# Performance work log

Measured on AMD Instinct MI355X. Metric: run time of the kernel, lower is better.

The kernel has to match this reference:

```python
import jax, jax.numpy as jnp
import numpy as np
import math

B, S, HID, H = 8, 512, 1024, 16
D = HID // H
ATT_SPAN = 512  # max_position_embeddings


def setup_inputs() -> dict:
    key = jax.random.key(0)
    ks = jax.random.split(key, 12)
    sd = 0.02
    hidden_states = jax.random.normal(ks[0], (B, S, HID), jnp.float32)
    attention_mask = jnp.zeros((B, 1, 1, S), jnp.float32)
    # DeBERTa build_relative_position: rel[i, j] = i - j, shape [1, 1, S, S]
    rel = (jnp.arange(S)[:, None] - jnp.arange(S)[None, :]).astype(jnp.int32)
    relative_pos = rel[None, None]
    Wq = jax.random.normal(ks[1], (HID, HID), jnp.float32) * sd
    bq = jnp.zeros((HID,), jnp.float32)
    Wk = jax.random.normal(ks[2], (HID, HID), jnp.float32) * sd
    bk = jnp.zeros((HID,), jnp.float32)
    Wv = jax.random.normal(ks[3], (HID, HID), jnp.float32) * sd
    bv = jnp.zeros((HID,), jnp.float32)
    Wpk = jax.random.normal(ks[4], (HID, HID), jnp.float32) * sd
    bpk = jnp.zeros((HID,), jnp.float32)
    rel_emb = jax.random.normal(ks[5], (2 * ATT_SPAN, HID), jnp.float32) * sd
    return dict(hidden_states=hidden_states, attention_mask=attention_mask,
                relative_pos=relative_pos, Wq=Wq, bq=bq, Wk=Wk, bk=bk,
                Wv=Wv, bv=bv, Wpk=Wpk, bpk=bpk, rel_emb=rel_emb)


def _fwd(hidden_states, attention_mask, relative_pos, Wq, bq, Wk, bk, Wv, bv, Wpk, bpk, rel_emb):
    b, s, _ = hidden_states.shape

    def proj(x, W, bias):  # [b,s,hid] -> [b,h,s,d]
        return (x @ W.T + bias).reshape(b, s, H, D).transpose(0, 2, 1, 3)

    q = proj(hidden_states, Wq, bq)
    k = proj(hidden_states, Wk, bk)
    v = proj(hidden_states, Wv, bv)

    # content-to-content scores, scaled by sqrt(3*num_heads) as in source
    s_content = jnp.einsum('bhid,bhjd->bhij', q, k) / math.sqrt(3.0 * H)

    # positional projections (source uses pos_key layer for BOTH key and query)
    # rel_emb: [2*ATT_SPAN, HID] -> [H, 2*ATT_SPAN, D]
    pos = (rel_emb @ Wpk.T + bpk).reshape(2 * ATT_SPAN, H, D).transpose(1, 0, 2)

    # c2p: q @ pos^T / sqrt(all_head_size * 3), then gather along last axis
    c2p_full = jnp.einsum('bhid,hpd->bhip', q, pos) / math.sqrt(HID * 3.0)  # [b,h,s,2P]
    c2p_pos = jnp.clip(relative_pos + ATT_SPAN, 0, 2 * ATT_SPAN - 1)
    c2p_pos = jnp.broadcast_to(c2p_pos, (b, H, s, s)).astype(jnp.int32)
    c2p = jnp.take_along_axis(c2p_full, c2p_pos, axis=-1)  # [b,h,s,s]

    # p2c: pos / sqrt(3*H) @ k^T, gather along dim -2 with same index
    p2c_full = jnp.einsum('hpd,bhjd->bhpj', pos / math.sqrt(3.0 * H), k)  # [b,h,2P,s]
    p2c = jnp.take_along_axis(p2c_full, c2p_pos, axis=-2)  # [b,h,s,s]

    score = s_content + c2p + p2c + attention_mask
    probs = jax.nn.softmax(score, axis=-1)  # dropout is identity in eval
    out = jnp.einsum('bhij,bhjd->bhid', probs, v)
    return out.transpose(0, 2, 1, 3).reshape(b, s, HID)


def reference(hidden_states, attention_mask, relative_pos, Wq, bq, Wk, bk, Wv, bv, Wpk, bpk, rel_emb):
    return _fwd(hidden_states, attention_mask, relative_pos, Wq, bq, Wk, bk, Wv, bv, Wpk, bpk, rel_emb)
```

## Files before the change

kernel.cpp:

```cpp
#include <hip/hip_runtime.h>
#include <cstdint>
#include <cstddef>

static constexpr int NB  = 8;
static constexpr int S   = 512;
static constexpr int HID = 1024;
static constexpr int NH  = 16;
static constexpr int DH  = 64;
static constexpr int P2  = 1024;

static constexpr float INV_S1 = 0.14433756729740643f;

typedef __bf16 v8bf  __attribute__((ext_vector_type(8)));
typedef __bf16 v4bf  __attribute__((ext_vector_type(4)));
typedef float  f32x4 __attribute__((ext_vector_type(4)));

#define MFMA16(acc, a, b) acc = __builtin_amdgcn_mfma_f32_16x16x32_bf16(a, b, acc, 0, 0, 0)

#define GLOAD_LDS16(gp, lp) __builtin_amdgcn_global_load_lds( \
    (const __attribute__((address_space(1))) void*)(gp), \
    (__attribute__((address_space(3))) void*)(lp), 16, 0, 0)

__global__ void castall(const float* __restrict__ x,  const float* __restrict__ wq,
                        const float* __restrict__ wk, const float* __restrict__ wv,
                        const float* __restrict__ wpk, const float* __restrict__ rel,
                        __bf16* __restrict__ ob) {
  size_t e = ((size_t)blockIdx.x * 256 + threadIdx.x) * 4;
  if (e >= 9437184) return;
  const float* src; size_t off;
  if (e < 4194304) { src = x; off = e; }
  else {
    int r = (int)((e - 4194304) >> 20);
    off = (e - 4194304) & 1048575;
    src = (r == 0) ? wq : (r == 1) ? wk : (r == 2) ? wv : (r == 3) ? wpk : rel;
  }
  float4 v = *(const float4*)(src + off);
  v4bf o;
  o[0] = (__bf16)v.x; o[1] = (__bf16)v.y; o[2] = (__bf16)v.z; o[3] = (__bf16)v.w;
  *(v4bf*)(ob + e) = o;
}

__launch_bounds__(256, 4)
__global__ void proj_gemm(const __bf16* __restrict__ Xb, const __bf16* __restrict__ Rb,
                          const __bf16* __restrict__ Wqb, const __bf16* __restrict__ Wkb,
                          const __bf16* __restrict__ Wvb, const __bf16* __restrict__ Wpkb,
                          const float* __restrict__ bq, const float* __restrict__ bk_,
                          const float* __restrict__ bv_, const float* __restrict__ bpk,
                          __bf16* __restrict__ qo, __bf16* __restrict__ ko,
                          __bf16* __restrict__ vto, __bf16* __restrict__ po) {
  const int z = blockIdx.z;
  const __bf16* A; const __bf16* W; const float* bias; __bf16* out; int M; float osc;
  if      (z == 0) { A = Xb; W = Wqb;  bias = bq;  out = qo;  M = 4096; osc = INV_S1; }
  else if (z == 1) { A = Xb; W = Wkb;  bias = bk_; out = ko;  M = 4096; osc = 1.0f; }
  else if (z == 2) { A = Xb; W = Wvb;  bias = bv_; out = vto; M = 4096; osc = 1.0f; }
  else             { A = Rb; W = Wpkb; bias = bpk; out = po;  M = 1024; osc = INV_S1; }
  const int m0 = blockIdx.x * 128;
  if (m0 >= M) return;
  const int n0 = blockIdx.y * 128;
  const int K = 1024;

  __shared__ __bf16 Al[128 * 64];
  __shared__ __bf16 Bl[128 * 64];

  const int t = threadIdx.x;
  const int w = t >> 6, lane = t & 63, q4 = lane >> 4, cc = lane & 15;
  const int wm = w >> 1, wn = w & 1;
  const int srow_in = lane >> 3;
  const int sseg    = ((lane & 7) ^ srow_in) * 8;

  f32x4 acc[4][4] = {};

  for (int k0 = 0; k0 < K; k0 += 64) {
    __syncthreads();
    #pragma unroll
    for (int i = 0; i < 4; i++) {
      int rr = w * 32 + i * 8;
      int gr = rr + srow_in;
      GLOAD_LDS16(&A[(size_t)(m0 + gr) * K + k0 + sseg], &Al[rr * 64]);
      GLOAD_LDS16(&W[(size_t)(n0 + gr) * K + k0 + sseg], &Bl[rr * 64]);
    }
    __syncthreads();
    #pragma unroll
    for (int kk = 0; kk < 2; kk++) {
      v8bf af[4], bfg[4];
      const int phys = ((4 * kk + q4) ^ (cc & 7)) * 8;
      #pragma unroll
      for (int mt = 0; mt < 4; mt++)
        af[mt] = *(const v8bf*)(&Al[(wm * 64 + mt * 16 + cc) * 64 + phys]);
      #pragma unroll
      for (int nt = 0; nt < 4; nt++)
        bfg[nt] = *(const v8bf*)(&Bl[(wn * 64 + nt * 16 + cc) * 64 + phys]);
      #pragma unroll
      for (int mt = 0; mt < 4; mt++)
        #pragma unroll
        for (int nt = 0; nt < 4; nt++)
          MFMA16(acc[mt][nt], af[mt], bfg[nt]);
    }
  }

  #pragma unroll
  for (int mt = 0; mt < 4; mt++) {
    #pragma unroll
    for (int nt = 0; nt < 4; nt++) {
      int n = n0 + wn * 64 + nt * 16 + cc;
      float bsv = bias[n];
      if (z == 2) {
        int m_base = m0 + wm * 64 + mt * 16 + q4 * 4;
        int bb = m_base >> 9, ss = m_base & 511, hh = n >> 6, dd = n & 63;
        v4bf st;
        st[0] = (__bf16)(acc[mt][nt][0] + bsv);
        st[1] = (__bf16)(acc[mt][nt][1] + bsv);
        st[2] = (__bf16)(acc[mt][nt][2] + bsv);
        st[3] = (__bf16)(acc[mt][nt][3] + bsv);
        *(v4bf*)(&out[(((size_t)bb * 16 + hh) * 64 + dd) * 512 + ss]) = st;
      } else {
        #pragma unroll
        for (int r = 0; r < 4; r++) {
          int m = m0 + wm * 64 + mt * 16 + q4 * 4 + r;
          float val = (acc[mt][nt][r] + bsv) * osc;
          size_t idx;
          if (z < 2)
            idx = ((size_t)(m >> 9) * 16 + (n >> 6)) * (512 * 64) + (size_t)(m & 511) * 64 + (n & 63);
          else
            idx = (size_t)(n >> 6) * (1024 * 64) + (size_t)m * 64 + (n & 63);
          out[idx] = (__bf16)val;
        }
      }
    }
  }
}

__launch_bounds__(256, 4)
__global__ void attn(const __bf16* __restrict__ qb, const __bf16* __restrict__ kb,
                     const __bf16* __restrict__ vtb, const __bf16* __restrict__ posb,
                     const float* __restrict__ mask,
                     float* __restrict__ out) {
  const int bh = blockIdx.y, b = bh >> 4, h = bh & 15;
  const int i0 = blockIdx.x * 64;

  __shared__ __bf16 Sb[64 * 136];

  const int t = threadIdx.x, w = t >> 6, lane = t & 63, q4 = lane >> 4, cc = lane & 15;
  const int arow = w * 16;
  const size_t bho = (size_t)bh * (S * DH);
  const __bf16* qp  = qb  + bho;
  const __bf16* kp  = kb  + bho;
  const __bf16* vtp = vtb + bho;
  const __bf16* pp  = posb + (size_t)h * (P2 * DH);

  v8bf aq0 = *(const v8bf*)(&qp[(size_t)(i0 + arow + cc) * DH + q4 * 8]);
  v8bf aq1 = *(const v8bf*)(&qp[(size_t)(i0 + arow + cc) * DH + 32 + q4 * 8]);

  f32x4 Oc[4] = {};
  float mrow[4], lrow[4];
  #pragma unroll
  for (int r = 0; r < 4; r++) { mrow[r] = -__builtin_inff(); lrow[r] = 0.f; }

#define LDP(d0, d1, U) { int p_ = pw0 + 16 * (U) + cc; p_ = min(max(p_, 0), P2 - 1); \
  const __bf16* pr_ = &pp[(size_t)p_ * DH + q4 * 8]; \
  d0 = *(const v8bf*)pr_; d1 = *(const v8bf*)(pr_ + 32); }
#define LDK(d0, d1, NT) { const __bf16* kr_ = &kp[(size_t)(j0 + (NT) * 16 + cc) * DH + q4 * 8]; \
  d0 = *(const v8bf*)kr_; d1 = *(const v8bf*)(kr_ + 32); }
#define GT(U, P0, P1) { f32x4 g_ = {}; MFMA16(g_, aq0, P0); MFMA16(g_, aq1, P1); \
  _Pragma("unroll") for (int r_ = 0; r_ < 4; r_++) { \
    int jj_ = q4 * 4 + r_ - 16 * (U) - cc + 63; \
    if ((unsigned)jj_ < 64u) Sb[(arow + q4 * 4 + r_) * 136 + jj_ * 2] = (__bf16)(g_[r_] * 0.8660254f); } }
#define HT(U, NT, P0, P1, K0, K1) { f32x4 h_ = {}; MFMA16(h_, P0, K0); MFMA16(h_, P1, K1); \
  _Pragma("unroll") for (int r_ = 0; r_ < 4; r_++) { \
    int ar_ = 16 * (U) + q4 * 4 + r_ + 16 * (NT) + cc - 63; \
    if ((unsigned)ar_ < 16u) Sb[(arow + ar_) * 136 + (16 * (NT) + cc) * 2 + 1] = (__bf16)h_[r_]; } }
#define CT(NT, K0, K1) { f32x4 c_ = {}; MFMA16(c_, aq0, K0); MFMA16(c_, aq1, K1); accc[NT] = c_; }

  for (int jt = 0; jt < 8; jt++) {
    const int j0 = jt * 64;
    const int pw0 = i0 + arow - j0 + 449;

    float mk[4];
    #pragma unroll
    for (int nt = 0; nt < 4; nt++) mk[nt] = mask[(size_t)b * S + j0 + nt * 16 + cc];

    f32x4 accc[4];
    v8bf p40,p41,p30,p31,p20,p21,p10,p11,p00,p01;
    v8bf k00,k01,k10,k11,k20,k21,k30,k31;

    LDP(p40, p41, 4); LDK(k00, k01, 0);
    LDP(p30, p31, 3); LDK(k10, k11, 1);
    GT(4, p40, p41); HT(4, 0, p40, p41, k00, k01); CT(0, k00, k01);
    LDP(p20, p21, 2); LDK(k20, k21, 2);
    GT(3, p30, p31); HT(3, 0, p30, p31, k00, k01); HT(3, 1, p30, p31, k10, k11); CT(1, k10, k11);
    LDP(p10, p11, 1); LDK(k30, k31, 3);
    GT(2, p20, p21); HT(2, 1, p20, p21, k10, k11); HT(2, 2, p20, p21, k20, k21); CT(2, k20, k21);
    LDP(p00, p01, 0);
    GT(1, p10, p11); HT(1, 2, p10, p11, k20, k21); HT(1, 3, p10, p11, k30, k31); CT(3, k30, k31);
    GT(0, p00, p01); HT(0, 3, p00, p01, k30, k31);

    float sc[4][4];
    float tmax[4] = { -__builtin_inff(), -__builtin_inff(), -__builtin_inff(), -__builtin_inff() };
    #pragma unroll
    for (int nt = 0; nt < 4; nt++) {
      int jj = nt * 16 + cc;
      #pragma unroll
      for (int r = 0; r < 4; r++) {
        const __bf16* slot = &Sb[(arow + q4 * 4 + r) * 136 + jj * 2];
        float s = accc[nt][r] + (float)slot[0] + (float)slot[1] + mk[nt];
        sc[nt][r] = s;
        tmax[r] = fmaxf(tmax[r], s);
      }
    }
    #pragma unroll
    for (int off = 1; off < 16; off <<= 1)
      #pragma unroll
      for (int r = 0; r < 4; r++) tmax[r] = fmaxf(tmax[r], __shfl_xor(tmax[r], off, 64));

    v8bf vf[2][4];
    #pragma unroll
    for (int kk = 0; kk < 2; kk++)
      #pragma unroll
      for (int dt = 0; dt < 4; dt++)
        vf[kk][dt] = *(const v8bf*)(&vtp[(size_t)(dt * 16 + cc) * S + j0 + kk * 32 + q4 * 8]);

    float alpha[4], psum[4];
    #pragma unroll
    for (int r = 0; r < 4; r++) {
      float mnew = fmaxf(mrow[r], tmax[r]);
      alpha[r] = __expf(mrow[r] - mnew);
      mrow[r] = mnew;
      psum[r] = 0.f;
    }
    #pragma unroll
    for (int nt = 0; nt < 4; nt++)
      #pragma unroll
      for (int r = 0; r < 4; r++) {
        float p = __expf(sc[nt][r] - mrow[r]);
        psum[r] += p;
        Sb[(arow + q4 * 4 + r) * 136 + nt * 16 + cc] = (__bf16)p;
      }
    #pragma unroll
    for (int off = 1; off < 16; off <<= 1)
      #pragma unroll
      for (int r = 0; r < 4; r++) psum[r] += __shfl_xor(psum[r], off, 64);
    #pragma unroll
    for (int r = 0; r < 4; r++) lrow[r] = lrow[r] * alpha[r] + psum[r];
    #pragma unroll
    for (int dt = 0; dt < 4; dt++)
      #pragma unroll
      for (int r = 0; r < 4; r++) Oc[dt][r] *= alpha[r];

    #pragma unroll
    for (int kk = 0; kk < 2; kk++) {
      v8bf ap = *(const v8bf*)(&Sb[(arow + cc) * 136 + kk * 32 + q4 * 8]);
      #pragma unroll
      for (int dt = 0; dt < 4; dt++)
        MFMA16(Oc[dt], ap, vf[kk][dt]);
    }
  }

  #pragma unroll
  for (int r = 0; r < 4; r++) {
    int i = i0 + arow + q4 * 4 + r;
    float rl = 1.0f / lrow[r];
    float* orow = &out[((size_t)b * S + i) * HID + h * 64];
    #pragma unroll
    for (int dt = 0; dt < 4; dt++)
      orow[dt * 16 + cc] = Oc[dt][r] * rl;
  }
#undef LDP
#undef LDK
#undef GT
#undef HT
#undef CT
}

extern "C" void kernel_launch(void* const* d_in, const int* in_sizes, int n_in,
                              void* d_out, int out_size, void* d_ws, size_t ws_size,
                              hipStream_t stream) {
  const float* hs   = (const float*)d_in[0];
  const float* mask = (const float*)d_in[1];
  const float* Wq  = (const float*)d_in[3];
  const float* bq  = (const float*)d_in[4];
  const float* Wk  = (const float*)d_in[5];
  const float* bk  = (const float*)d_in[6];
  const float* Wv  = (const float*)d_in[7];
  const float* bv  = (const float*)d_in[8];
  const float* Wpk = (const float*)d_in[9];
  const float* bpk = (const float*)d_in[10];
  const float* rel = (const float*)d_in[11];
  float* out = (float*)d_out;

  char* ws = (char*)d_ws;
  __bf16* cb   = (__bf16*)ws;
  __bf16* Xb   = cb;
  __bf16* Wqb  = cb + 4194304;
  __bf16* Wkb  = cb + 5242880;
  __bf16* Wvb  = cb + 6291456;
  __bf16* Wpkb = cb + 7340032;
  __bf16* Rb   = cb + 8388608;
  __bf16* qb   = (__bf16*)(ws + 18874368);
  __bf16* kb   = (__bf16*)(ws + 27262976);
  __bf16* vtb  = (__bf16*)(ws + 35651584);
  __bf16* posb = (__bf16*)(ws + 44040192);

  castall<<<9216, 256, 0, stream>>>(hs, Wq, Wk, Wv, Wpk, rel, cb);

  proj_gemm<<<dim3(32, 8, 4), 256, 0, stream>>>(Xb, Rb, Wqb, Wkb, Wvb, Wpkb,
                                                bq, bk, bv, bpk, qb, kb, vtb, posb);

  attn<<<dim3(8, 128), 256, 0, stream>>>(qb, kb, vtb, posb, mask, out);
}
```

Before: 248.8 us.

## Stage K and V tiles through swizzled LDS with register prefetch

Each 64-key tile of K and transposed V is loaded once per block into registers, then written into XOR-swizzled shared memory. All four waves read their MFMA operands from LDS instead of each wave fetching the same K/V rows from global memory. The next tile is prefetched into registers while the current tile is being computed. This cuts redundant global/L2 traffic, but adds two block-wide barriers per tile, 16 KB of extra LDS that could lower occupancy, and some register pressure.

```diff
diff --git a/kernel.cpp b/kernel.cpp
--- a/kernel.cpp
+++ b/kernel.cpp
@@ -139,6 +139,8 @@
   const int i0 = blockIdx.x * 64;
 
   __shared__ __bf16 Sb[64 * 136];
+  __shared__ __bf16 Kl[64 * 64];
+  __shared__ __bf16 Vl[64 * 64];
 
   const int t = threadIdx.x, w = t >> 6, lane = t & 63, q4 = lane >> 4, cc = lane & 15;
   const int arow = w * 16;
@@ -148,6 +150,12 @@
   const __bf16* vtp = vtb + bho;
   const __bf16* pp  = posb + (size_t)h * (P2 * DH);
 
+  const int str0 = t >> 3;
+  const int scs  = (t & 7) ^ (str0 & 7);
+  const int pch  = (t & 7) * 8;
+  const int swA = (q4       ^ (cc & 7)) * 8;
+  const int swB = ((q4 + 4) ^ (cc & 7)) * 8;
+
   v8bf aq0 = *(const v8bf*)(&qp[(size_t)(i0 + arow + cc) * DH + q4 * 8]);
   v8bf aq1 = *(const v8bf*)(&qp[(size_t)(i0 + arow + cc) * DH + 32 + q4 * 8]);
 
@@ -156,11 +164,22 @@
   #pragma unroll
   for (int r = 0; r < 4; r++) { mrow[r] = -__builtin_inff(); lrow[r] = 0.f; }
 
+  int4 kst0, kst1, vst0, vst1;
+#define STAGE_LOAD(J0) { \
+  const __bf16* kq_ = &kp[(size_t)((J0) + str0) * 64 + scs * 8]; \
+  kst0 = *(const int4*)kq_; kst1 = *(const int4*)(kq_ + 32 * 64); \
+  const __bf16* vq_ = &vtp[(size_t)str0 * 512 + (J0) + scs * 8]; \
+  vst0 = *(const int4*)vq_; vst1 = *(const int4*)(vq_ + 32 * 512); }
+#define STAGE_WRITE() { \
+  *(int4*)(&Kl[str0 * 64 + pch]) = kst0; *(int4*)(&Kl[(str0 + 32) * 64 + pch]) = kst1; \
+  *(int4*)(&Vl[str0 * 64 + pch]) = vst0; *(int4*)(&Vl[(str0 + 32) * 64 + pch]) = vst1; }
+
 #define LDP(d0, d1, U) { int p_ = pw0 + 16 * (U) + cc; p_ = min(max(p_, 0), P2 - 1); \
   const __bf16* pr_ = &pp[(size_t)p_ * DH + q4 * 8]; \
   d0 = *(const v8bf*)pr_; d1 = *(const v8bf*)(pr_ + 32); }
-#define LDK(d0, d1, NT) { const __bf16* kr_ = &kp[(size_t)(j0 + (NT) * 16 + cc) * DH + q4 * 8]; \
-  d0 = *(const v8bf*)kr_; d1 = *(const v8bf*)(kr_ + 32); }
+#define LDK(d0, d1, NT) { const int rr_ = ((NT) * 16 + cc) * 64; \
+  d0 = *(const v8bf*)(&Kl[rr_ + swA]); \
+  d1 = *(const v8bf*)(&Kl[rr_ + swB]); }
 #define GT(U, P0, P1) { f32x4 g_ = {}; MFMA16(g_, aq0, P0); MFMA16(g_, aq1, P1); \
   _Pragma("unroll") for (int r_ = 0; r_ < 4; r_++) { \
     int jj_ = q4 * 4 + r_ - 16 * (U) - cc + 63; \
@@ -171,9 +190,16 @@
     if ((unsigned)ar_ < 16u) Sb[(arow + ar_) * 136 + (16 * (NT) + cc) * 2 + 1] = (__bf16)h_[r_]; } }
 #define CT(NT, K0, K1) { f32x4 c_ = {}; MFMA16(c_, aq0, K0); MFMA16(c_, aq1, K1); accc[NT] = c_; }
 
+  STAGE_LOAD(0);
+
   for (int jt = 0; jt < 8; jt++) {
     const int j0 = jt * 64;
     const int pw0 = i0 + arow - j0 + 449;
+
+    __syncthreads();
+    STAGE_WRITE();
+    __syncthreads();
+    if (jt < 7) STAGE_LOAD(j0 + 64);
 
     float mk[4];
     #pragma unroll
@@ -217,7 +243,7 @@
     for (int kk = 0; kk < 2; kk++)
       #pragma unroll
       for (int dt = 0; dt < 4; dt++)
-        vf[kk][dt] = *(const v8bf*)(&vtp[(size_t)(dt * 16 + cc) * S + j0 + kk * 32 + q4 * 8]);
+        vf[kk][dt] = *(const v8bf*)(&Vl[(dt * 16 + cc) * 64 + (kk ? swB : swA)]);
 
     float alpha[4], psum[4];
     #pragma unroll
@@ -269,6 +295,8 @@
 #undef GT
 #undef HT
 #undef CT
+#undef STAGE_LOAD
+#undef STAGE_WRITE
 }
 
 extern "C" void kernel_launch(void* const* d_in, const int* in_sizes, int n_in,
```

Result: slower. 267.6 us (+7.5%).

## Double-buffer K/pos tile prefetch and add lazy softmax max rescaling

Applied to the files above, without the earlier changes.

The attention loop now runs two tiles per iteration with ping-pong register sets, so the K fragments and first pos fragment for the next 64-column tile are loaded while the current tile's scores are still being processed. It also adds a lazy online-softmax rescale: the cross-lane max reduction and the rescaling of the accumulator and row sums only happen when some row's new max exceeds the running max by more than 8. This removes shuffles and multiplies from most iterations, at the cost of higher register pressure and exponentials that can grow up to e^8 before a rescale.

```diff
diff --git a/kernel.cpp b/kernel.cpp
--- a/kernel.cpp
+++ b/kernel.cpp
@@ -156,10 +156,10 @@
   #pragma unroll
   for (int r = 0; r < 4; r++) { mrow[r] = -__builtin_inff(); lrow[r] = 0.f; }
 
-#define LDP(d0, d1, U) { int p_ = pw0 + 16 * (U) + cc; p_ = min(max(p_, 0), P2 - 1); \
+#define LDPN(d0, d1, PW) { int p_ = (PW) + cc; p_ = min(max(p_, 0), P2 - 1); \
   const __bf16* pr_ = &pp[(size_t)p_ * DH + q4 * 8]; \
   d0 = *(const v8bf*)pr_; d1 = *(const v8bf*)(pr_ + 32); }
-#define LDK(d0, d1, NT) { const __bf16* kr_ = &kp[(size_t)(j0 + (NT) * 16 + cc) * DH + q4 * 8]; \
+#define LDKJ(d0, d1, NT, J) { const __bf16* kr_ = &kp[(size_t)((J) + (NT) * 16 + cc) * DH + q4 * 8]; \
   d0 = *(const v8bf*)kr_; d1 = *(const v8bf*)(kr_ + 32); }
 #define GT(U, P0, P1) { f32x4 g_ = {}; MFMA16(g_, aq0, P0); MFMA16(g_, aq1, P1); \
   _Pragma("unroll") for (int r_ = 0; r_ < 4; r_++) { \
@@ -171,88 +171,91 @@
     if ((unsigned)ar_ < 16u) Sb[(arow + ar_) * 136 + (16 * (NT) + cc) * 2 + 1] = (__bf16)h_[r_]; } }
 #define CT(NT, K0, K1) { f32x4 c_ = {}; MFMA16(c_, aq0, K0); MFMA16(c_, aq1, K1); accc[NT] = c_; }
 
-  for (int jt = 0; jt < 8; jt++) {
-    const int j0 = jt * 64;
-    const int pw0 = i0 + arow - j0 + 449;
-
-    float mk[4];
-    #pragma unroll
-    for (int nt = 0; nt < 4; nt++) mk[nt] = mask[(size_t)b * S + j0 + nt * 16 + cc];
-
-    f32x4 accc[4];
-    v8bf p40,p41,p30,p31,p20,p21,p10,p11,p00,p01;
-    v8bf k00,k01,k10,k11,k20,k21,k30,k31;
-
-    LDP(p40, p41, 4); LDK(k00, k01, 0);
-    LDP(p30, p31, 3); LDK(k10, k11, 1);
-    GT(4, p40, p41); HT(4, 0, p40, p41, k00, k01); CT(0, k00, k01);
-    LDP(p20, p21, 2); LDK(k20, k21, 2);
-    GT(3, p30, p31); HT(3, 0, p30, p31, k00, k01); HT(3, 1, p30, p31, k10, k11); CT(1, k10, k11);
-    LDP(p10, p11, 1); LDK(k30, k31, 3);
-    GT(2, p20, p21); HT(2, 1, p20, p21, k10, k11); HT(2, 2, p20, p21, k20, k21); CT(2, k20, k21);
-    LDP(p00, p01, 0);
-    GT(1, p10, p11); HT(1, 2, p10, p11, k20, k21); HT(1, 3, p10, p11, k30, k31); CT(3, k30, k31);
-    GT(0, p00, p01); HT(0, 3, p00, p01, k30, k31);
-
-    float sc[4][4];
-    float tmax[4] = { -__builtin_inff(), -__builtin_inff(), -__builtin_inff(), -__builtin_inff() };
-    #pragma unroll
-    for (int nt = 0; nt < 4; nt++) {
-      int jj = nt * 16 + cc;
-      #pragma unroll
-      for (int r = 0; r < 4; r++) {
-        const __bf16* slot = &Sb[(arow + q4 * 4 + r) * 136 + jj * 2];
-        float s = accc[nt][r] + (float)slot[0] + (float)slot[1] + mk[nt];
-        sc[nt][r] = s;
-        tmax[r] = fmaxf(tmax[r], s);
-      }
-    }
-    #pragma unroll
-    for (int off = 1; off < 16; off <<= 1)
-      #pragma unroll
-      for (int r = 0; r < 4; r++) tmax[r] = fmaxf(tmax[r], __shfl_xor(tmax[r], off, 64));
-
-    v8bf vf[2][4];
-    #pragma unroll
-    for (int kk = 0; kk < 2; kk++)
-      #pragma unroll
-      for (int dt = 0; dt < 4; dt++)
-        vf[kk][dt] = *(const v8bf*)(&vtp[(size_t)(dt * 16 + cc) * S + j0 + kk * 32 + q4 * 8]);
-
-    float alpha[4], psum[4];
-    #pragma unroll
-    for (int r = 0; r < 4; r++) {
-      float mnew = fmaxf(mrow[r], tmax[r]);
-      alpha[r] = __expf(mrow[r] - mnew);
-      mrow[r] = mnew;
-      psum[r] = 0.f;
-    }
-    #pragma unroll
-    for (int nt = 0; nt < 4; nt++)
-      #pragma unroll
-      for (int r = 0; r < 4; r++) {
-        float p = __expf(sc[nt][r] - mrow[r]);
-        psum[r] += p;
-        Sb[(arow + q4 * 4 + r) * 136 + nt * 16 + cc] = (__bf16)p;
-      }
-    #pragma unroll
-    for (int off = 1; off < 16; off <<= 1)
-      #pragma unroll
-      for (int r = 0; r < 4; r++) psum[r] += __shfl_xor(psum[r], off, 64);
-    #pragma unroll
-    for (int r = 0; r < 4; r++) lrow[r] = lrow[r] * alpha[r] + psum[r];
-    #pragma unroll
-    for (int dt = 0; dt < 4; dt++)
-      #pragma unroll
-      for (int r = 0; r < 4; r++) Oc[dt][r] *= alpha[r];
-
-    #pragma unroll
-    for (int kk = 0; kk < 2; kk++) {
-      v8bf ap = *(const v8bf*)(&Sb[(arow + cc) * 136 + kk * 32 + q4 * 8]);
-      #pragma unroll
-      for (int dt = 0; dt < 4; dt++)
-        MFMA16(Oc[dt], ap, vf[kk][dt]);
-    }
+  v8bf kA00,kA01,kA10,kA11,kA20,kA21,kA30,kA31;
+  v8bf kB00,kB01,kB10,kB11,kB20,kB21,kB30,kB31;
+  v8bf pn0, pn1;
+
+  LDKJ(kA00,kA01,0,0); LDKJ(kA10,kA11,1,0); LDKJ(kA20,kA21,2,0); LDKJ(kA30,kA31,3,0);
+  LDPN(pn0, pn1, i0 + arow + 449 + 64);
+
+#define ATTN_BODY(J0, kc00,kc01,kc10,kc11,kc20,kc21,kc30,kc31, \
+                      kn00,kn01,kn10,kn11,kn20,kn21,kn30,kn31) { \
+    const int j0 = (J0); \
+    const int pw0 = i0 + arow - j0 + 449; \
+    float mk[4]; \
+    _Pragma("unroll") for (int nt = 0; nt < 4; nt++) \
+      mk[nt] = mask[(size_t)b * S + j0 + nt * 16 + cc]; \
+    f32x4 accc[4]; \
+    v8bf p30,p31,p20,p21,p10,p11,p00,p01; \
+    LDPN(p30, p31, pw0 + 48); \
+    GT(4, pn0, pn1); HT(4, 0, pn0, pn1, kc00, kc01); CT(0, kc00, kc01); \
+    LDPN(p20, p21, pw0 + 32); \
+    GT(3, p30, p31); HT(3, 0, p30, p31, kc00, kc01); HT(3, 1, p30, p31, kc10, kc11); CT(1, kc10, kc11); \
+    LDPN(p10, p11, pw0 + 16); \
+    GT(2, p20, p21); HT(2, 1, p20, p21, kc10, kc11); HT(2, 2, p20, p21, kc20, kc21); CT(2, kc20, kc21); \
+    LDPN(p00, p01, pw0); \
+    GT(1, p10, p11); HT(1, 2, p10, p11, kc20, kc21); HT(1, 3, p10, p11, kc30, kc31); CT(3, kc30, kc31); \
+    GT(0, p00, p01); HT(0, 3, p00, p01, kc30, kc31); \
+     \
+    { const int jn_ = (j0 + 64 <= 448) ? (j0 + 64) : 448; \
+      LDKJ(kn00, kn01, 0, jn_); LDKJ(kn10, kn11, 1, jn_); \
+      LDKJ(kn20, kn21, 2, jn_); LDKJ(kn30, kn31, 3, jn_); \
+      LDPN(pn0, pn1, pw0);  } \
+    float sc[4][4]; \
+    _Pragma("unroll") for (int nt = 0; nt < 4; nt++) { \
+      int jj = nt * 16 + cc; \
+      _Pragma("unroll") for (int r = 0; r < 4; r++) { \
+        const __bf16* slot = &Sb[(arow + q4 * 4 + r) * 136 + jj * 2]; \
+        sc[nt][r] = accc[nt][r] + (float)slot[0] + (float)slot[1] + mk[nt]; \
+      } \
+    } \
+    float tl[4]; \
+    _Pragma("unroll") for (int r = 0; r < 4; r++) \
+      tl[r] = fmaxf(fmaxf(sc[0][r], sc[1][r]), fmaxf(sc[2][r], sc[3][r])); \
+    float dmax = tl[0] - mrow[0]; \
+    _Pragma("unroll") for (int r = 1; r < 4; r++) dmax = fmaxf(dmax, tl[r] - mrow[r]); \
+    if (__any(dmax > 8.0f)) { \
+      float tmax[4]; \
+      _Pragma("unroll") for (int r = 0; r < 4; r++) tmax[r] = tl[r]; \
+      _Pragma("unroll") for (int off = 1; off < 16; off <<= 1) \
+        _Pragma("unroll") for (int r = 0; r < 4; r++) \
+          tmax[r] = fmaxf(tmax[r], __shfl_xor(tmax[r], off, 64)); \
+      _Pragma("unroll") for (int r = 0; r < 4; r++) { \
+        float mnew = fmaxf(mrow[r], tmax[r]); \
+        float alpha = __expf(mrow[r] - mnew); \
+        mrow[r] = mnew; \
+        lrow[r] *= alpha; \
+        _Pragma("unroll") for (int dt = 0; dt < 4; dt++) Oc[dt][r] *= alpha; \
+      } \
+    } \
+    v8bf vf[2][4]; \
+    _Pragma("unroll") for (int kk = 0; kk < 2; kk++) \
+      _Pragma("unroll") for (int dt = 0; dt < 4; dt++) \
+        vf[kk][dt] = *(const v8bf*)(&vtp[(size_t)(dt * 16 + cc) * S + j0 + kk * 32 + q4 * 8]); \
+    float psum[4] = { 0.f, 0.f, 0.f, 0.f }; \
+    _Pragma("unroll") for (int nt = 0; nt < 4; nt++) \
+      _Pragma("unroll") for (int r = 0; r < 4; r++) { \
+        float p = __expf(sc[nt][r] - mrow[r]); \
+        psum[r] += p; \
+        Sb[(arow + q4 * 4 + r) * 136 + nt * 16 + cc] = (__bf16)p; \
+      } \
+    _Pragma("unroll") for (int off = 1; off < 16; off <<= 1) \
+      _Pragma("unroll") for (int r = 0; r < 4; r++) psum[r] += __shfl_xor(psum[r], off, 64); \
+    _Pragma("unroll") for (int r = 0; r < 4; r++) lrow[r] += psum[r]; \
+    _Pragma("unroll") for (int kk = 0; kk < 2; kk++) { \
+      v8bf ap = *(const v8bf*)(&Sb[(arow + cc) * 136 + kk * 32 + q4 * 8]); \
+      _Pragma("unroll") for (int dt = 0; dt < 4; dt++) \
+        MFMA16(Oc[dt], ap, vf[kk][dt]); \
+    } \
+  }
+
+  for (int j2 = 0; j2 < 512; j2 += 128) {
+    ATTN_BODY(j2,
+              kA00,kA01,kA10,kA11,kA20,kA21,kA30,kA31,
+              kB00,kB01,kB10,kB11,kB20,kB21,kB30,kB31);
+    ATTN_BODY(j2 + 64,
+              kB00,kB01,kB10,kB11,kB20,kB21,kB30,kB31,
+              kA00,kA01,kA10,kA11,kA20,kA21,kA30,kA31);
   }
 
   #pragma unroll
@@ -264,8 +267,9 @@
     for (int dt = 0; dt < 4; dt++)
       orow[dt * 16 + cc] = Oc[dt][r] * rl;
   }
-#undef LDP
-#undef LDK
+#undef ATTN_BODY
+#undef LDPN
+#undef LDKJ
 #undef GT
 #undef HT
 #undef CT
```

Result: slower. 339.9 us (+36.6%).
